# Performance work log

Measured on AMD Instinct MI355X. Metric: run time of the kernel, lower is better.

## Reference

```python
import jax, jax.numpy as jnp
import numpy as np
from jax import lax

D_MODEL = 512
D_STATE = 64
D_CONV = 4
EXPAND = 2
HEADDIM = 64
D_INNER = EXPAND * D_MODEL          # 1024
NHEADS = D_INNER // HEADDIM         # 16
CONV_DIM = D_INNER + 2 * D_STATE    # 1152 (x, B, C go through depthwise conv)
D_PROJ = 2 * D_INNER + 2 * D_STATE + NHEADS  # 2192
EPS = 1e-5


def silu(x):
    return x * jax.nn.sigmoid(x)


def layernorm(x, w, b):
    mu = jnp.mean(x, axis=-1, keepdims=True)
    var = jnp.mean((x - mu) ** 2, axis=-1, keepdims=True)
    return (x - mu) * lax.rsqrt(var + EPS) * w + b


def mamba2(x, in_w, conv_w, conv_b, dt_bias, A_log, D_h, mnorm_w, out_w):
    """Faithful Mamba2 forward (sequential selective-scan form of SSD).
    x: [B, L, D_MODEL]"""
    Bsz, L, _ = x.shape
    zxbcdt = x @ in_w  # [B, L, D_PROJ]
    z = zxbcdt[..., :D_INNER]
    xBC = zxbcdt[..., D_INNER:D_INNER + CONV_DIM]
    dt = zxbcdt[..., -NHEADS:]

    # causal depthwise conv1d over sequence, then SiLU
    xBC_pad = jnp.pad(xBC, ((0, 0), (D_CONV - 1, 0), (0, 0)))
    xBC = lax.conv_general_dilated(
        xBC_pad, conv_w, window_strides=(1,), padding='VALID',
        dimension_numbers=('NWC', 'WIO', 'NWC'), feature_group_count=CONV_DIM)
    xBC = silu(xBC + conv_b)

    xh = xBC[..., :D_INNER].reshape(Bsz, L, NHEADS, HEADDIM)      # [B,L,H,P]
    Bc = xBC[..., D_INNER:D_INNER + D_STATE]                      # [B,L,N]
    Cc = xBC[..., D_INNER + D_STATE:]                             # [B,L,N]

    dt = jax.nn.softplus(dt + dt_bias)          # [B,L,H]
    dA = jnp.exp(dt * (-jnp.exp(A_log)))        # [B,L,H]
    dtx = dt[..., None] * xh                    # [B,L,H,P]

    def step(h, ins):
        dA_t, dtx_t, B_t, C_t = ins  # [B,H], [B,H,P], [B,N], [B,N]
        h = h * dA_t[:, :, None, None] + dtx_t[..., None] * B_t[:, None, None, :]
        y = jnp.einsum('bhpn,bn->bhp', h, C_t)
        return h, y

    h0 = jnp.zeros((Bsz, NHEADS, HEADDIM, D_STATE), x.dtype)
    xs = (jnp.moveaxis(dA, 1, 0), jnp.moveaxis(dtx, 1, 0),
          jnp.moveaxis(Bc, 1, 0), jnp.moveaxis(Cc, 1, 0))
    _, ys = lax.scan(step, h0, xs)              # [L,B,H,P]
    y = jnp.moveaxis(ys, 0, 1) + D_h[None, None, :, None] * xh
    y = y.reshape(Bsz, L, D_INNER)

    # gated RMSNorm: rmsnorm(y * silu(z)) * weight
    g = y * silu(z)
    g = g * lax.rsqrt(jnp.mean(g * g, axis=-1, keepdims=True) + EPS) * mnorm_w
    return g @ out_w  # [B, L, D_MODEL]


def setup_inputs() -> dict:
    key = jax.random.key(0)
    ks = jax.random.split(key, 16)
    B, L = 2, 4096
    s = 0.02
    inp = {
        'x': jax.random.normal(ks[0], (B, L, D_MODEL), jnp.float32),
        'norm_in_w': jnp.ones((D_MODEL,), jnp.float32),
        'norm_in_b': jnp.zeros((D_MODEL,), jnp.float32),
        'norm_out_w': jnp.ones((D_MODEL,), jnp.float32),
        'norm_out_b': jnp.zeros((D_MODEL,), jnp.float32),
        'in_w': jax.random.normal(ks[1], (D_MODEL, D_PROJ), jnp.float32) * s,
        'conv_w': jax.random.normal(ks[2], (D_CONV, 1, CONV_DIM), jnp.float32) * 0.1,
        'conv_b': jnp.zeros((CONV_DIM,), jnp.float32),
        'dt_bias': jnp.log(jnp.expm1(jax.random.uniform(ks[3], (NHEADS,), jnp.float32, 0.001, 0.1))),
        'A_log': jnp.log(jnp.arange(1, NHEADS + 1, dtype=jnp.float32)),
        'D_h': jnp.ones((NHEADS,), jnp.float32),
        'mnorm_w': jnp.ones((D_INNER,), jnp.float32),
        'out_w': jax.random.normal(ks[4], (D_INNER, D_MODEL), jnp.float32) * s,
        'ff_w1': jax.random.normal(ks[5], (D_MODEL, 4 * D_MODEL), jnp.float32) * s,
        'ff_b1': jnp.zeros((4 * D_MODEL,), jnp.float32),
        'ff_w2': jax.random.normal(ks[6], (4 * D_MODEL, D_MODEL), jnp.float32) * s,
        'ff_b2': jnp.zeros((D_MODEL,), jnp.float32),
    }
    return inp


def reference(x, norm_in_w, norm_in_b, norm_out_w, norm_out_b, in_w, conv_w,
              conv_b, dt_bias, A_log, D_h, mnorm_w, out_w, ff_w1, ff_b1,
              ff_w2, ff_b2):
    xn = layernorm(x, norm_in_w, norm_in_b)
    fwd = mamba2(xn, in_w, conv_w, conv_b, dt_bias, A_log, D_h, mnorm_w, out_w)
    bwd = mamba2(jnp.flip(xn, axis=1), in_w, conv_w, conv_b, dt_bias, A_log,
                 D_h, mnorm_w, out_w)
    m = layernorm(fwd + jnp.flip(bwd, axis=1), norm_out_w, norm_out_b)
    ff = jax.nn.gelu(m @ ff_w1 + ff_b1, approximate=False) @ ff_w2 + ff_b2
    return ff + x
```

## Files before the change

kernel.cpp:

```cpp
#include <hip/hip_runtime.h>
#include <hip/hip_bf16.h>

#define LSEQ 4096
#define BSZ 2
#define DMODEL 512
#define DINNER 1024
#define DSTATE 64
#define NHEADS 16
#define CONVDIM 1152
#define DPROJ 2192
#define NPAD 2304
#define NTOK (BSZ*LSEQ)
#define NCH 64

typedef __attribute__((ext_vector_type(8))) short short8;
typedef __attribute__((ext_vector_type(4))) float f32x4;

__device__ inline unsigned short f2b(float v){
  unsigned int u = __builtin_bit_cast(unsigned int, v);
  unsigned int r = (u + 0x7FFFu + ((u >> 16) & 1u)) >> 16;
  return (unsigned short)r;
}
__device__ inline float b2f(unsigned short u){
  unsigned int x = ((unsigned int)u) << 16;
  return __builtin_bit_cast(float, x);
}
__device__ inline uint4 pack8(const float* v){
  uint4 pk;
  pk.x = (unsigned)f2b(v[0]) | ((unsigned)f2b(v[1])<<16);
  pk.y = (unsigned)f2b(v[2]) | ((unsigned)f2b(v[3])<<16);
  pk.z = (unsigned)f2b(v[4]) | ((unsigned)f2b(v[5])<<16);
  pk.w = (unsigned)f2b(v[6]) | ((unsigned)f2b(v[7])<<16);
  return pk;
}
__device__ inline float gelu_f(float x){
  float x2 = x*x;
  float u = x*(0.7978845608f + 0.0356774081f*x2);
  float au = fabsf(u);
  float z = __expf(-2.f*au);
  float t = (1.f - z)/(1.f + z);
  t = (u >= 0.f) ? t : -t;
  return 0.5f*x*(1.f + t);
}

#define GLL16(gp, lp) __builtin_amdgcn_global_load_lds( \
    (const __attribute__((address_space(1))) unsigned int*)(gp), \
    (__attribute__((address_space(3))) unsigned int*)(lp), 16, 0, 0)

__global__ __launch_bounds__(256) void wconv_t(const float* __restrict__ src,
    unsigned short* __restrict__ dst, int K, int Nsrc, int Npad){
  __shared__ float t[32][33];
  int n0 = blockIdx.x*32, k0 = blockIdx.y*32;
  int tx = threadIdx.x & 31, ty = threadIdx.x >> 5;
  for (int i=0;i<4;i++){
    int k = k0 + ty + i*8; int n = n0 + tx;
    t[ty + i*8][tx] = (n < Nsrc) ? src[(size_t)k*Nsrc + n] : 0.f;
  }
  __syncthreads();
  for (int i=0;i<4;i++){
    int n = n0 + ty + i*8; int k = k0 + tx;
    if (n < Npad) dst[(size_t)n*K + k] = f2b(t[tx][ty + i*8]);
  }
}

__global__ __launch_bounds__(256) void layernorm_k(const float* __restrict__ in,
    const float* __restrict__ w, const float* __restrict__ bb, unsigned short* __restrict__ out){
  int row = blockIdx.x; int tid = threadIdx.x;
  const float* r = in + (size_t)row*DMODEL;
  float v0 = r[tid], v1 = r[tid+256];
  float s = v0+v1, sq = v0*v0+v1*v1;
  for (int m=32;m>=1;m>>=1){ s += __shfl_xor(s,m); sq += __shfl_xor(sq,m); }
  __shared__ float ws_[4], wq_[4];
  int wave = tid>>6, lane = tid&63;
  if (lane==0){ ws_[wave]=s; wq_[wave]=sq; }
  __syncthreads();
  s = ws_[0]+ws_[1]+ws_[2]+ws_[3]; sq = wq_[0]+wq_[1]+wq_[2]+wq_[3];
  float mu = s * (1.f/DMODEL);
  float var = sq * (1.f/DMODEL) - mu*mu;
  float rs = rsqrtf(var + 1e-5f);
  out[(size_t)row*DMODEL + tid]     = f2b((v0-mu)*rs*w[tid] + bb[tid]);
  out[(size_t)row*DMODEL + tid+256] = f2b((v1-mu)*rs*w[tid+256] + bb[tid+256]);
}

__global__ __launch_bounds__(256) void layernorm4_k(const float* __restrict__ in0,
    const float* __restrict__ in1, const float* __restrict__ in2, const float* __restrict__ in3,
    const float* __restrict__ w, const float* __restrict__ bb, unsigned short* __restrict__ out){
  int row = blockIdx.x; int tid = threadIdx.x;
  size_t o = (size_t)row*DMODEL;
  float v0 = in0[o+tid] + in1[o+tid] + in2[o+tid] + in3[o+tid];
  float v1 = in0[o+tid+256] + in1[o+tid+256] + in2[o+tid+256] + in3[o+tid+256];
  float s = v0+v1, sq = v0*v0+v1*v1;
  for (int m=32;m>=1;m>>=1){ s += __shfl_xor(s,m); sq += __shfl_xor(sq,m); }
  __shared__ float ws_[4], wq_[4];
  int wave = tid>>6, lane = tid&63;
  if (lane==0){ ws_[wave]=s; wq_[wave]=sq; }
  __syncthreads();
  s = ws_[0]+ws_[1]+ws_[2]+ws_[3]; sq = wq_[0]+wq_[1]+wq_[2]+wq_[3];
  float mu = s * (1.f/DMODEL);
  float var = sq * (1.f/DMODEL) - mu*mu;
  float rs = rsqrtf(var + 1e-5f);
  out[o + tid]     = f2b((v0-mu)*rs*w[tid] + bb[tid]);
  out[o + tid+256] = f2b((v1-mu)*rs*w[tid+256] + bb[tid+256]);
}

__global__ __launch_bounds__(256) void reduce4_k(const float* __restrict__ pa,
    const float* __restrict__ pb, const float* __restrict__ bias,
    const float* __restrict__ resid, float* __restrict__ out){
  const size_t MN4 = (size_t)NTOK*DMODEL/4;
  for (size_t i = (size_t)blockIdx.x*256 + threadIdx.x; i < MN4; i += (size_t)gridDim.x*256){
    float4 a0 = ((const float4*)pa)[i];
    float4 a1 = ((const float4*)pa)[i + MN4];
    float4 b0 = ((const float4*)pb)[i];
    float4 b1 = ((const float4*)pb)[i + MN4];
    float4 rv = ((const float4*)resid)[i];
    int col = (int)((i*4) & (DMODEL-1));
    const float4 bs = *(const float4*)(bias + col);
    float4 o;
    o.x = a0.x + a1.x + b0.x + b1.x + bs.x + rv.x;
    o.y = a0.y + a1.y + b0.y + b1.y + bs.y + rv.y;
    o.z = a0.z + a1.z + b0.z + b1.z + bs.z + rv.z;
    o.w = a0.w + a1.w + b0.w + b1.w + bs.w + rv.w;
    ((float4*)out)[i] = o;
  }
}

__global__ __launch_bounds__(512, 4) void gemm128_k(const unsigned short* __restrict__ A,
    const unsigned short* __restrict__ Bt, void* __restrict__ outp, void* __restrict__ outp_hi,
    int M, int N, int K, int klen, int epi, const float* __restrict__ bias){
  __shared__ __align__(16) unsigned short sm[24576];
  unsigned short* As = sm;
  unsigned short* Bs = sm + 8192;
  const int tid = threadIdx.x;
  const int lane = tid & 63, wave = tid >> 6;
  const int wr = wave >> 2, wc = wave & 3;
  const int l15 = lane & 15, q = lane >> 4;
  int nbx = gridDim.x;
  int bid = blockIdx.y * nbx + blockIdx.x;
  int cpx = (nbx * gridDim.y) >> 3;
  int swz = (bid & 7) * cpx + (bid >> 3);
  int bn = swz % nbx, bm = swz / nbx;
  const int kstart = blockIdx.z * klen;
  const int NT = klen >> 5;
  const int ra  = tid >> 2;
  const int sca = (tid & 3) ^ ((ra >> 1) & 3);
  const int jb1 = tid + 512;
  const int rb1 = jb1 >> 2;
  const int scb1 = (jb1 & 3) ^ ((rb1 >> 1) & 3);
  const unsigned short* ga  = A  + (size_t)(bm*128 + ra )*K + kstart + sca*8;
  const unsigned short* gb0 = Bt + (size_t)(bn*256 + ra )*K + kstart + sca*8;
  const unsigned short* gb1 = Bt + (size_t)(bn*256 + rb1)*K + kstart + scb1*8;
  unsigned short* lAa = As + tid*8;
  unsigned short* lB0 = Bs + tid*8;
  unsigned short* lB1 = Bs + jb1*8;
#define STG(t) { const int go=(t)*32, loa=((t)&1)*4096, lob=((t)&1)*8192; \
  GLL16(ga+go, lAa+loa); GLL16(gb0+go, lB0+lob); GLL16(gb1+go, lB1+lob); }
  f32x4 acc[4][4];
  #pragma unroll
  for (int i=0;i<4;i++)
    #pragma unroll
    for (int j=0;j<4;j++) acc[i][j] = (f32x4){0.f,0.f,0.f,0.f};
  STG(0); STG(1);
  const int cOfs = (q ^ ((l15 >> 1) & 3)) * 8;
  const int arow = wr*64 + l15;
  const int brow = wc*64 + l15;
  for (int t = 0; t < NT; ++t){
    if (t+1 < NT) { asm volatile("s_waitcnt vmcnt(3)" ::: "memory"); }
    else          { asm volatile("s_waitcnt vmcnt(0)" ::: "memory"); }
    __builtin_amdgcn_s_barrier();
    const unsigned short* Ab = As + (t & 1)*4096;
    const unsigned short* Bb = Bs + (t & 1)*8192;
    short8 af[4], bf4[4];
    #pragma unroll
    for (int mt=0;mt<4;mt++) af[mt]  = *(const short8*)(Ab + (arow + mt*16)*32 + cOfs);
    #pragma unroll
    for (int nt=0;nt<4;nt++) bf4[nt] = *(const short8*)(Bb + (brow + nt*16)*32 + cOfs);
    __builtin_amdgcn_s_setprio(1);
    #pragma unroll
    for (int mt=0;mt<4;mt++)
      #pragma unroll
      for (int nt=0;nt<4;nt++)
        acc[mt][nt] = __builtin_amdgcn_mfma_f32_16x16x32_bf16(af[mt], bf4[nt], acc[mt][nt], 0,0,0);
    __builtin_amdgcn_s_setprio(0);
    __builtin_amdgcn_s_barrier();
    if (t+2 < NT) STG(t+2);
  }
#undef STG
  float* cb = (float*)sm + wave*1040;
  const int rbase = q*4;
  const int gr0t = bm*128 + wr*64;
  const int gc0 = bn*256 + wc*64;
  #pragma unroll
  for (int mt=0; mt<4; mt++){
    #pragma unroll
    for (int nt=0;nt<4;nt++)
      #pragma unroll
      for (int r=0;r<4;r++)
        cb[(rbase+r)*65 + nt*16 + l15] = acc[mt][nt][r];
    int gr0 = gr0t + mt*16;
    if (epi == 0){
      float* po = (float*)((blockIdx.z < 2) ? outp : outp_hi)
                + (size_t)(blockIdx.z & 1) * ((size_t)M * N);
      int r4 = lane >> 4, c0f = (lane & 15)*4;
      #pragma unroll
      for (int h=0; h<4; h++){
        int row = h*4 + r4;
        float4 v;
        v.x = cb[row*65 + c0f + 0];
        v.y = cb[row*65 + c0f + 1];
        v.z = cb[row*65 + c0f + 2];
        v.w = cb[row*65 + c0f + 3];
        *(float4*)(po + (size_t)(gr0+row)*N + gc0 + c0f) = v;
      }
    } else {
      int r8 = lane >> 3, c0 = (lane & 7)*8;
      #pragma unroll
      for (int h=0; h<2; h++){
        int row = h*8 + r8;
        float v[8];
        #pragma unroll
        for (int u=0;u<8;u++) v[u] = cb[row*65 + c0 + u];
        if (epi == 1){
          #pragma unroll
          for (int u=0;u<8;u++) v[u] = gelu_f(v[u] + bias[gc0 + c0 + u]);
        }
        *(uint4*)((unsigned short*)outp + (size_t)(gr0+row)*N + gc0 + c0) = pack8(v);
      }
    }
  }
}

__global__ __launch_bounds__(256) void dt_k(const unsigned short* __restrict__ zx,
    const float* __restrict__ dt_bias, const float* __restrict__ A_log,
    float* __restrict__ dAb, float* __restrict__ dtb){
  int b = blockIdx.y;
  int t = blockIdx.x*16 + (threadIdx.x>>4);
  int h = threadIdx.x & 15;
  float raw = b2f(zx[((size_t)b*LSEQ + t)*NPAD + (DINNER+CONVDIM) + h]) + dt_bias[h];
  float dt = (raw > 20.f) ? raw : log1pf(expf(raw));
  float dA = expf(-expf(A_log[h]) * dt);
  size_t f = ((size_t)b*LSEQ + t)*NHEADS + h;
  size_t r = ((size_t)(BSZ+b)*LSEQ + (LSEQ-1-t))*NHEADS + h;
  dAb[f] = dA; dtb[f] = dt;
  dAb[r] = dA; dtb[r] = dt;
}

__global__ __launch_bounds__(256) void conv_x_k(const unsigned short* __restrict__ zx,
    const float* __restrict__ conv_w, const float* __restrict__ conv_b,
    const float* __restrict__ dtb, unsigned short* __restrict__ dtxb,
    unsigned short* __restrict__ zcomp){
  int b = blockIdx.y;
  int t0blk = blockIdx.x * 32;
  int tid = threadIdx.x;
  int half = tid >> 7, cg = tid & 127;
  int c0 = cg * 8;
  int head = c0 >> 6;
  float wk[4][8], bias8[8];
  #pragma unroll
  for (int k=0;k<4;k++)
    #pragma unroll
    for (int j=0;j<8;j++) wk[k][j] = conv_w[k*CONVDIM + c0 + j];
  #pragma unroll
  for (int j=0;j<8;j++) bias8[j] = conv_b[c0 + j];
  __shared__ float sdtf[32][16], sdtb[32][16];
  for (int r = tid; r < 512; r += 256){
    int i = r >> 4, h = r & 15;
    sdtf[i][h] = dtb[((size_t)b*LSEQ + t0blk + i)*NHEADS + h];
    sdtb[i][h] = dtb[((size_t)(BSZ+b)*LSEQ + (LSEQ-1-(t0blk+i)))*NHEADS + h];
  }
  __syncthreads();
  int t0 = t0blk + half*16;
  float w0[8],w1[8],w2[8],w3[8];
  #pragma unroll
  for (int j=0;j<8;j++){ w1[j]=0.f; w2[j]=0.f; w3[j]=0.f; }
  for (int it=0; it<22; ++it){
    int t = t0 - 3 + it;
    #pragma unroll
    for (int j=0;j<8;j++){ w0[j]=w1[j]; w1[j]=w2[j]; w2[j]=w3[j]; }
    if (t >= 0 && t < LSEQ){
      uint4 xv = *(const uint4*)(zx + ((size_t)b*LSEQ + t)*NPAD + DINNER + c0);
      const unsigned short* xs = (const unsigned short*)&xv;
      #pragma unroll
      for (int j=0;j<8;j++) w3[j] = b2f(xs[j]);
      if (t >= t0 && t < t0+16){
        uint4 zv = *(const uint4*)(zx + ((size_t)b*LSEQ + t)*NPAD + c0);
        *(uint4*)(zcomp + ((size_t)b*LSEQ + t)*DINNER + c0) = zv;
      }
    } else {
      #pragma unroll
      for (int j=0;j<8;j++) w3[j] = 0.f;
    }
    if (t >= t0 && t < t0+16){
      float dtf = sdtf[t - t0blk][head];
      float v[8];
      #pragma unroll
      for (int j=0;j<8;j++){
        float a = bias8[j] + wk[0][j]*w0[j] + wk[1][j]*w1[j] + wk[2][j]*w2[j] + wk[3][j]*w3[j];
        v[j] = (a / (1.f + __expf(-a))) * dtf;
      }
      *(uint4*)(dtxb + ((size_t)b*LSEQ + t)*DINNER + c0) = pack8(v);
    }
    int tau = t - 3;
    if (tau >= t0 && tau < t0+16){
      float dtv = sdtb[tau - t0blk][head];
      float v[8];
      #pragma unroll
      for (int j=0;j<8;j++){
        float a = bias8[j] + wk[0][j]*w3[j] + wk[1][j]*w2[j] + wk[2][j]*w1[j] + wk[3][j]*w0[j];
        v[j] = (a / (1.f + __expf(-a))) * dtv;
      }
      *(uint4*)(dtxb + ((size_t)(BSZ+b)*LSEQ + (LSEQ-1-tau))*DINNER + c0) = pack8(v);
    }
  }
}

__global__ __launch_bounds__(256) void conv_bc_k(const unsigned short* __restrict__ zx,
    const float* __restrict__ conv_w, const float* __restrict__ conv_b,
    unsigned short* __restrict__ Bb, unsigned short* __restrict__ Cb){
  int b = blockIdx.y;
  int t0blk = blockIdx.x * 64;
  int tid = threadIdx.x;
  int slot = tid >> 4, cg = tid & 15;
  int c0 = cg*8;
  int ccol = DINNER + 1024 + c0;
  int cw = 1024 + c0;
  float wk[4][8], bias8[8];
  #pragma unroll
  for (int k=0;k<4;k++)
    #pragma unroll
    for (int j=0;j<8;j++) wk[k][j] = conv_w[k*CONVDIM + cw + j];
  #pragma unroll
  for (int j=0;j<8;j++) bias8[j] = conv_b[cw + j];
  int t0 = t0blk + slot*4;
  float w0[8],w1[8],w2[8],w3[8];
  #pragma unroll
  for (int j=0;j<8;j++){ w1[j]=0.f; w2[j]=0.f; w3[j]=0.f; }
  for (int it=0; it<10; ++it){
    int t = t0 - 3 + it;
    #pragma unroll
    for (int j=0;j<8;j++){ w0[j]=w1[j]; w1[j]=w2[j]; w2[j]=w3[j]; }
    if (t >= 0 && t < LSEQ){
      uint4 xv = *(const uint4*)(zx + ((size_t)b*LSEQ + t)*NPAD + ccol);
      const unsigned short* xs = (const unsigned short*)&xv;
      #pragma unroll
      for (int j=0;j<8;j++) w3[j] = b2f(xs[j]);
    } else {
      #pragma unroll
      for (int j=0;j<8;j++) w3[j] = 0.f;
    }
    if (t >= t0 && t < t0+4){
      float v[8];
      #pragma unroll
      for (int j=0;j<8;j++){
        float a = bias8[j] + wk[0][j]*w0[j] + wk[1][j]*w1[j] + wk[2][j]*w2[j] + wk[3][j]*w3[j];
        v[j] = a / (1.f + __expf(-a));
      }
      size_t tok = (size_t)b*LSEQ + t;
      if (c0 < 64) *(uint4*)(Bb + tok*DSTATE + c0)      = pack8(v);
      else         *(uint4*)(Cb + tok*DSTATE + (c0-64)) = pack8(v);
    }
    int tau = t - 3;
    if (tau >= t0 && tau < t0+4){
      float v[8];
      #pragma unroll
      for (int j=0;j<8;j++){
        float a = bias8[j] + wk[0][j]*w3[j] + wk[1][j]*w2[j] + wk[2][j]*w1[j] + wk[3][j]*w0[j];
        v[j] = a / (1.f + __expf(-a));
      }
      size_t tok = (size_t)(BSZ+b)*LSEQ + (LSEQ-1-tau);
      if (c0 < 64) *(uint4*)(Bb + tok*DSTATE + c0)      = pack8(v);
      else         *(uint4*)(Cb + tok*DSTATE + (c0-64)) = pack8(v);
    }
  }
}

template<int SA, int SB>
__device__ inline void gemm64s(const unsigned short* Ab, const unsigned short* Bb_,
                               int l15, int q, f32x4 acc[4][4]){
  #pragma unroll
  for (int ks=0; ks<2; ks++){
    short8 af[4], bf4[4];
    #pragma unroll
    for (int mt=0;mt<4;mt++){
      int r = mt*16 + l15;
      int c = ks*4 + q; if (SA) c ^= (r>>3)&7;
      af[mt] = *(const short8*)(Ab + r*72 + c*8);
    }
    #pragma unroll
    for (int nt=0;nt<4;nt++){
      int r = nt*16 + l15;
      int c = ks*4 + q; if (SB) c ^= (r>>3)&7;
      bf4[nt] = *(const short8*)(Bb_ + r*72 + c*8);
    }
    #pragma unroll
    for (int mt=0;mt<4;mt++)
      #pragma unroll
      for (int nt=0;nt<4;nt++)
        acc[mt][nt] = __builtin_amdgcn_mfma_f32_16x16x32_bf16(af[mt], bf4[nt], acc[mt][nt], 0,0,0);
  }
}
__device__ inline void gemm64(const unsigned short* Ab, const unsigned short* Bb_,
                              int l15, int q, f32x4 acc[4][4]){
  gemm64s<0,0>(Ab, Bb_, l15, q, acc);
}

__global__ __launch_bounds__(64) void ssd1_k(const float* __restrict__ dAb,
    const unsigned short* __restrict__ dtxb, const unsigned short* __restrict__ Bb,
    const unsigned short* __restrict__ Cb,
    unsigned short* __restrict__ y0, unsigned short* __restrict__ y1,
    unsigned short* __restrict__ hbuf, float* __restrict__ Pch, float* __restrict__ ebuf){
  int ch = blockIdx.x, h = blockIdx.y, z = blockIdx.z;
  int d = z >> 1, b = z & 1;
  int lane = threadIdx.x;
  int l15 = lane & 15, q = lane >> 4;
  int tr = lane >> 3, cb8 = (lane & 7)*8;
  int m7 = lane & 7;
  size_t tokb = (size_t)z*LSEQ + (size_t)ch*64;
  size_t zhc = ((size_t)z*NHEADS + h)*NCH + ch;
  __shared__ __align__(16) unsigned short S1[64*72];
  __shared__ __align__(16) unsigned short S2[64*72];
  __shared__ __align__(16) unsigned short S3[64*72];
  __shared__ float Lb[64];
  float L = fmaxf(logf(dAb[(tokb + lane)*NHEADS + h]), -60.f);
  #pragma unroll
  for (int off=1; off<64; off<<=1){
    float v = __shfl_up(L, off);
    if (lane >= off) L += v;
  }
  Lb[lane] = L;
  float e = __expf(L);
  ebuf[zhc*64 + lane] = e;
  if (lane == 63) Pch[zhc] = e;
  for (int i=0;i<8;i++){
    int t = i*8 + tr;
    *(uint4*)&S1[t*72 + cb8] = *(const uint4*)(Cb + (tokb+t)*DSTATE + cb8);
    *(uint4*)&S2[t*72 + cb8] = *(const uint4*)(Bb + (tokb+t)*DSTATE + cb8);
    uint4 xv = *(const uint4*)(dtxb + (tokb+t)*DINNER + (size_t)h*64 + cb8);
    const unsigned short* xs = (const unsigned short*)&xv;
    int csw = ((i ^ m7) << 3) + tr;
    #pragma unroll
    for (int j=0;j<8;j++) S3[(cb8+j)*72 + csw] = xs[j];
  }
  f32x4 sa[4][4];
  for (int i=0;i<4;i++) for (int j=0;j<4;j++) sa[i][j] = (f32x4){0.f,0.f,0.f,0.f};
  gemm64s<0,0>(S1, S2, l15, q, sa);
  float Lsv[4];
  #pragma unroll
  for (int nt=0;nt<4;nt++) Lsv[nt] = Lb[nt*16 + l15];
  int sch = l15 >> 3, sin = l15 & 7;
  #pragma unroll
  for (int mt=0;mt<4;mt++){
    #pragma unroll
    for (int r=0;r<4;r++){
      int t = mt*16 + q*4 + r;
      int trow = (t>>3)&7;
      float Lt = Lb[t];
      #pragma unroll
      for (int nt=0;nt<4;nt++){
        int s = nt*16 + l15;
        float v = (t >= s) ? __expf(Lt - Lsv[nt]) * sa[mt][nt][r] : 0.f;
        S1[t*72 + (((nt*2 + sch) ^ trow)<<3) + sin] = f2b(v);
      }
    }
  }
  f32x4 ya[4][4];
  for (int i=0;i<4;i++) for (int j=0;j<4;j++) ya[i][j] = (f32x4){0.f,0.f,0.f,0.f};
  gemm64s<1,1>(S1, S3, l15, q, ya);
  #pragma unroll
  for (int mt=0;mt<4;mt++)
    #pragma unroll
    for (int pt=0;pt<4;pt++)
      #pragma unroll
      for (int r=0;r<4;r++)
        S2[(mt*16+q*4+r)*72 + pt*16 + l15] = f2b(ya[mt][pt][r]);
  unsigned short* yb = d ? y1 : y0;
  for (int i=0;i<8;i++){
    int t = i*8 + tr; int g = ch*64 + t;
    int tph = d ? (LSEQ-1-g) : g;
    *(uint4*)(yb + ((size_t)b*LSEQ + tph)*DINNER + (size_t)h*64 + cb8) = *(uint4*)&S2[t*72 + cb8];
  }
  float L63 = Lb[63];
  for (int i=0;i<8;i++){
    int s = i*8 + tr;
    float w = __expf(L63 - Lb[s]);
    uint4 bv = *(const uint4*)(Bb + (tokb+s)*DSTATE + cb8);
    const unsigned short* bs = (const unsigned short*)&bv;
    int csw = ((i ^ m7) << 3) + tr;
    #pragma unroll
    for (int j=0;j<8;j++) S2[(cb8+j)*72 + csw] = f2b(w * b2f(bs[j]));
  }
  f32x4 ga[4][4];
  for (int i=0;i<4;i++) for (int j=0;j<4;j++) ga[i][j] = (f32x4){0.f,0.f,0.f,0.f};
  gemm64s<1,1>(S3, S2, l15, q, ga);
  #pragma unroll
  for (int pt=0;pt<4;pt++)
    #pragma unroll
    for (int nt=0;nt<4;nt++)
      #pragma unroll
      for (int r=0;r<4;r++)
        S1[(pt*16+q*4+r)*72 + nt*16 + l15] = f2b(ga[pt][nt][r]);
  for (int i=0;i<8;i++){
    int p = i*8 + tr;
    *(uint4*)(hbuf + zhc*4096 + (size_t)p*64 + cb8) = *(uint4*)&S1[p*72 + cb8];
  }
}

__global__ __launch_bounds__(256) void comb_k(unsigned short* __restrict__ hbuf,
    const float* __restrict__ Pch){
  int u = blockIdx.x; int tid = threadIdx.x;
  int kb = blockIdx.y * 4;
  size_t base0 = ((size_t)u*NCH)*4096;
  float hreg[4];
  unsigned short ccur[4], cnxt[4] = {0,0,0,0};
  #pragma unroll
  for (int k=0;k<4;k++){ hreg[k]=0.f; ccur[k] = hbuf[base0 + tid + (size_t)(kb+k)*256]; }
  float Pc = Pch[(size_t)u*NCH], Pn = 0.f;
  for (int ch=0; ch<NCH; ch++){
    size_t base = base0 + (size_t)ch*4096;
    if (ch+1 < NCH){
      size_t bnx = base + 4096;
      #pragma unroll
      for (int k=0;k<4;k++) cnxt[k] = hbuf[bnx + tid + (size_t)(kb+k)*256];
      Pn = Pch[(size_t)u*NCH + ch + 1];
    }
    #pragma unroll
    for (int k=0;k<4;k++){
      hbuf[base + tid + (size_t)(kb+k)*256] = f2b(hreg[k]);
      hreg[k] = hreg[k]*Pc + b2f(ccur[k]);
    }
    #pragma unroll
    for (int k=0;k<4;k++) ccur[k] = cnxt[k];
    Pc = Pn;
  }
}

__global__ __launch_bounds__(64) void ssd2_k(const unsigned short* __restrict__ Cb,
    const unsigned short* __restrict__ hbuf, const unsigned short* __restrict__ dtxb,
    const float* __restrict__ dtb, const float* __restrict__ ebuf, const float* __restrict__ Dh,
    unsigned short* __restrict__ y0, unsigned short* __restrict__ y1){
  int ch = blockIdx.x, h = blockIdx.y, z = blockIdx.z;
  int d = z >> 1, b = z & 1;
  int lane = threadIdx.x;
  int l15 = lane & 15, q = lane >> 4;
  int tr = lane >> 3, cb8 = (lane & 7)*8;
  size_t tokb = (size_t)z*LSEQ + (size_t)ch*64;
  size_t zhc = ((size_t)z*NHEADS + h)*NCH + ch;
  __shared__ __align__(16) unsigned short S1[64*72];
  __shared__ __align__(16) unsigned short S2[64*72];
  __shared__ __align__(16) unsigned short S3[64*72];
  __shared__ float eb2[64], dti[64];
  eb2[lane] = ebuf[zhc*64 + lane];
  dti[lane] = 1.f / dtb[(tokb + lane)*NHEADS + h];
  float Dv = Dh[h];
  for (int i=0;i<8;i++){
    int t = i*8 + tr;
    *(uint4*)&S1[t*72 + cb8] = *(const uint4*)(Cb + (tokb+t)*DSTATE + cb8);
    *(uint4*)&S2[t*72 + cb8] = *(const uint4*)(hbuf + zhc*4096 + (size_t)t*64 + cb8);
  }
  f32x4 acc[4][4];
  for (int i=0;i<4;i++) for (int j=0;j<4;j++) acc[i][j] = (f32x4){0.f,0.f,0.f,0.f};
  gemm64(S1, S2, l15, q, acc);
  unsigned short* yb = d ? y1 : y0;
  #pragma unroll
  for (int mt=0;mt<4;mt++){
    #pragma unroll
    for (int r=0;r<4;r++){
      int t = mt*16 + q*4 + r; int g = ch*64 + t;
      int tph = d ? (LSEQ-1-g) : g;
      size_t rowb = ((size_t)b*LSEQ + tph)*DINNER + (size_t)h*64;
      size_t dxb_ = (tokb + t)*DINNER + (size_t)h*64;
      float et = eb2[t], di = dti[t];
      #pragma unroll
      for (int pt=0;pt<4;pt++){
        int p = pt*16 + l15;
        float v = acc[mt][pt][r]*et + b2f(yb[rowb + p]) + Dv * b2f(dtxb[dxb_ + p]) * di;
        S3[t*72 + p] = f2b(v);
      }
    }
  }
  for (int i=0;i<8;i++){
    int t = i*8 + tr; int g = ch*64 + t;
    int tph = d ? (LSEQ-1-g) : g;
    *(uint4*)(yb + ((size_t)b*LSEQ + tph)*DINNER + (size_t)h*64 + cb8) = *(uint4*)&S3[t*72 + cb8];
  }
}

__global__ __launch_bounds__(256) void gate_k(const unsigned short* __restrict__ y0,
    const unsigned short* __restrict__ y1, const unsigned short* __restrict__ zcomp,
    const float* __restrict__ mnw, unsigned short* __restrict__ gsum){
  int tok = blockIdx.x; int tid = threadIdx.x;
  __shared__ float g0s[DINNER], g1s[DINNER];
  float ss0 = 0.f, ss1 = 0.f;
  for (int i=0;i<4;i++){
    int c = tid + i*256;
    float z = b2f(zcomp[(size_t)tok*DINNER + c]);
    float sz = z / (1.f + __expf(-z));
    float g0 = b2f(y0[(size_t)tok*DINNER + c]) * sz;
    float g1 = b2f(y1[(size_t)tok*DINNER + c]) * sz;
    g0s[c] = g0; g1s[c] = g1;
    ss0 += g0*g0; ss1 += g1*g1;
  }
  for (int m=32;m>=1;m>>=1){ ss0 += __shfl_xor(ss0,m); ss1 += __shfl_xor(ss1,m); }
  __shared__ float w0[4], w1[4];
  int wave = tid>>6, lane = tid&63;
  if (lane==0){ w0[wave]=ss0; w1[wave]=ss1; }
  __syncthreads();
  ss0 = w0[0]+w0[1]+w0[2]+w0[3];
  ss1 = w1[0]+w1[1]+w1[2]+w1[3];
  float r0 = rsqrtf(ss0*(1.f/DINNER) + 1e-5f);
  float r1 = rsqrtf(ss1*(1.f/DINNER) + 1e-5f);
  for (int i=0;i<4;i++){
    int c = tid + i*256;
    gsum[(size_t)tok*DINNER + c] = f2b((g0s[c]*r0 + g1s[c]*r1) * mnw[c]);
  }
}

extern "C" void kernel_launch(void* const* d_in, const int* in_sizes, int n_in,
                              void* d_out, int out_size, void* d_ws, size_t ws_size,
                              hipStream_t stream){
  const float* x       = (const float*)d_in[0];
  const float* nin_w   = (const float*)d_in[1];
  const float* nin_b   = (const float*)d_in[2];
  const float* nout_w  = (const float*)d_in[3];
  const float* nout_b  = (const float*)d_in[4];
  const float* in_w    = (const float*)d_in[5];
  const float* conv_w  = (const float*)d_in[6];
  const float* conv_b  = (const float*)d_in[7];
  const float* dt_bias = (const float*)d_in[8];
  const float* A_log   = (const float*)d_in[9];
  const float* D_h     = (const float*)d_in[10];
  const float* mnorm_w = (const float*)d_in[11];
  const float* out_w   = (const float*)d_in[12];
  const float* ff_w1   = (const float*)d_in[13];
  const float* ff_b1   = (const float*)d_in[14];
  const float* ff_w2   = (const float*)d_in[15];
  const float* ff_b2   = (const float*)d_in[16];
  float* out = (float*)d_out;

  char* ws = (char*)d_ws;
  size_t off = 0;
  auto alloc = [&](size_t bytes)->char*{
    char* p = ws + off; off = (off + bytes + 255) & ~(size_t)255; return p; };
  unsigned short* xn_bf = (unsigned short*)alloc((size_t)NTOK*DMODEL*2);
  unsigned short* in_wT = (unsigned short*)alloc((size_t)NPAD*DMODEL*2);
  unsigned short* out_wT= (unsigned short*)alloc((size_t)DMODEL*DINNER*2);
  unsigned short* w1T   = (unsigned short*)alloc((size_t)2048*DMODEL*2);
  unsigned short* w2T   = (unsigned short*)alloc((size_t)DMODEL*2048*2);
  unsigned short* zx    = (unsigned short*)alloc((size_t)NTOK*NPAD*2);
  unsigned short* zcomp = (unsigned short*)alloc((size_t)NTOK*DINNER*2);
  float*          dAb   = (float*)alloc((size_t)2*NTOK*NHEADS*4);
  float*          dtb   = (float*)alloc((size_t)2*NTOK*NHEADS*4);
  unsigned short* Bb    = (unsigned short*)alloc((size_t)2*NTOK*DSTATE*2);
  unsigned short* Cb    = (unsigned short*)alloc((size_t)2*NTOK*DSTATE*2);
  unsigned short* dtxb  = (unsigned short*)alloc((size_t)2*NTOK*DINNER*2);
  unsigned short* y0    = (unsigned short*)alloc((size_t)NTOK*DINNER*2);
  unsigned short* y1    = (unsigned short*)alloc((size_t)NTOK*DINNER*2);
  float*          Pch   = (float*)alloc((size_t)64*NCH*4);
  float*          ebuf  = (float*)alloc((size_t)64*NCH*64*4);
  size_t need = off;
  if (need > ws_size) return;

  unsigned short* hbuf  = zx;
  unsigned short* gsum  = dtxb;
  float* mp01 = (float*)zx;
  float* mp23 = (float*)y0;
  unsigned short* m_bf  = xn_bf;
  unsigned short* h1    = zx;
  float* fp01 = (float*)dtxb;
  float* fp23 = (float*)y0;

  wconv_t<<<dim3(NPAD/32,   DMODEL/32), 256, 0, stream>>>(in_w,  in_wT,  DMODEL, DPROJ,  NPAD);
  wconv_t<<<dim3(DMODEL/32, DINNER/32), 256, 0, stream>>>(out_w, out_wT, DINNER, DMODEL, DMODEL);
  wconv_t<<<dim3(2048/32,   DMODEL/32), 256, 0, stream>>>(ff_w1, w1T,    DMODEL, 2048,   2048);
  wconv_t<<<dim3(DMODEL/32, 2048/32),   256, 0, stream>>>(ff_w2, w2T,    2048,   DMODEL, DMODEL);
  layernorm_k<<<NTOK, 256, 0, stream>>>(x, nin_w, nin_b, xn_bf);
  gemm128_k<<<dim3(NPAD/256, NTOK/128, 1), 512, 0, stream>>>(xn_bf, in_wT, zx, nullptr, NTOK, NPAD, DMODEL, DMODEL, 3, nullptr);
  dt_k<<<dim3(LSEQ/16, BSZ), 256, 0, stream>>>(zx, dt_bias, A_log, dAb, dtb);
  conv_x_k<<<dim3(LSEQ/32, BSZ), 256, 0, stream>>>(zx, conv_w, conv_b, dtb, dtxb, zcomp);
  conv_bc_k<<<dim3(LSEQ/64, BSZ), 256, 0, stream>>>(zx, conv_w, conv_b, Bb, Cb);
  ssd1_k<<<dim3(NCH, NHEADS, 2*BSZ), 64, 0, stream>>>(dAb, dtxb, Bb, Cb, y0, y1, hbuf, Pch, ebuf);
  comb_k<<<dim3(64, 4), 256, 0, stream>>>(hbuf, Pch);
  ssd2_k<<<dim3(NCH, NHEADS, 2*BSZ), 64, 0, stream>>>(Cb, hbuf, dtxb, dtb, ebuf, D_h, y0, y1);
  gate_k<<<NTOK, 256, 0, stream>>>(y0, y1, zcomp, mnorm_w, gsum);
  gemm128_k<<<dim3(DMODEL/256, NTOK/128, 4), 512, 0, stream>>>(gsum, out_wT, mp01, mp23, NTOK, DMODEL, DINNER, 256, 0, nullptr);
  layernorm4_k<<<NTOK, 256, 0, stream>>>(mp01, mp01 + (size_t)NTOK*DMODEL, mp23, mp23 + (size_t)NTOK*DMODEL, nout_w, nout_b, m_bf);
  gemm128_k<<<dim3(2048/256, NTOK/128, 1), 512, 0, stream>>>(m_bf, w1T, h1, nullptr, NTOK, 2048, DMODEL, DMODEL, 1, ff_b1);
  gemm128_k<<<dim3(DMODEL/256, NTOK/128, 4), 512, 0, stream>>>(h1, w2T, fp01, fp23, NTOK, DMODEL, 2048, 512, 0, nullptr);
  reduce4_k<<<2048, 256, 0, stream>>>(fp01, fp23, ff_b2, x, out);
}
```

Measured before the change: 398.7 us.

## Split SSD chunk kernels across four wavefronts per block

The intra-chunk SSD kernels ssd1_k and ssd2_k move from one 64-lane wavefront per block to four wavefronts. Each wave computes one 16-column slice of every 64x64 MFMA product, and the loads and stores are shared across waves, with __syncthreads between stages. This cuts the per-wave accumulator registers and serial work, so each chunk has more parallelism and more latency hiding. In exchange it adds barrier overhead and the waves reload the A fragments redundantly.

```diff
diff --git a/kernel.cpp b/kernel.cpp
--- a/kernel.cpp
+++ b/kernel.cpp
@@ -374,43 +374,37 @@
 }
 
 template<int SA, int SB>
-__device__ inline void gemm64s(const unsigned short* Ab, const unsigned short* Bb_,
-                               int l15, int q, f32x4 acc[4][4]){
+__device__ inline void gemm64w(const unsigned short* Ab, const unsigned short* Bb_,
+                               int l15, int q, int nt, f32x4 acc[4]){
   #pragma unroll
   for (int ks=0; ks<2; ks++){
-    short8 af[4], bf4[4];
+    short8 af[4], bf;
     #pragma unroll
     for (int mt=0;mt<4;mt++){
       int r = mt*16 + l15;
       int c = ks*4 + q; if (SA) c ^= (r>>3)&7;
       af[mt] = *(const short8*)(Ab + r*72 + c*8);
     }
-    #pragma unroll
-    for (int nt=0;nt<4;nt++){
+    {
       int r = nt*16 + l15;
       int c = ks*4 + q; if (SB) c ^= (r>>3)&7;
-      bf4[nt] = *(const short8*)(Bb_ + r*72 + c*8);
+      bf = *(const short8*)(Bb_ + r*72 + c*8);
     }
     #pragma unroll
     for (int mt=0;mt<4;mt++)
-      #pragma unroll
-      for (int nt=0;nt<4;nt++)
-        acc[mt][nt] = __builtin_amdgcn_mfma_f32_16x16x32_bf16(af[mt], bf4[nt], acc[mt][nt], 0,0,0);
-  }
-}
-__device__ inline void gemm64(const unsigned short* Ab, const unsigned short* Bb_,
-                              int l15, int q, f32x4 acc[4][4]){
-  gemm64s<0,0>(Ab, Bb_, l15, q, acc);
-}
-
-__global__ __launch_bounds__(64) void ssd1_k(const float* __restrict__ dAb,
+      acc[mt] = __builtin_amdgcn_mfma_f32_16x16x32_bf16(af[mt], bf, acc[mt], 0,0,0);
+  }
+}
+
+__global__ __launch_bounds__(256) void ssd1_k(const float* __restrict__ dAb,
     const unsigned short* __restrict__ dtxb, const unsigned short* __restrict__ Bb,
     const unsigned short* __restrict__ Cb,
     unsigned short* __restrict__ y0, unsigned short* __restrict__ y1,
     unsigned short* __restrict__ hbuf, float* __restrict__ Pch, float* __restrict__ ebuf){
   int ch = blockIdx.x, h = blockIdx.y, z = blockIdx.z;
   int d = z >> 1, b = z & 1;
-  int lane = threadIdx.x;
+  int tid = threadIdx.x;
+  int lane = tid & 63, w = tid >> 6;
   int l15 = lane & 15, q = lane >> 4;
   int tr = lane >> 3, cb8 = (lane & 7)*8;
   int m7 = lane & 7;
@@ -426,12 +420,15 @@
     float v = __shfl_up(L, off);
     if (lane >= off) L += v;
   }
-  Lb[lane] = L;
-  float e = __expf(L);
-  ebuf[zhc*64 + lane] = e;
-  if (lane == 63) Pch[zhc] = e;
-  for (int i=0;i<8;i++){
-    int t = i*8 + tr;
+  if (w == 0){
+    Lb[lane] = L;
+    float e = __expf(L);
+    ebuf[zhc*64 + lane] = e;
+    if (lane == 63) Pch[zhc] = e;
+  }
+  #pragma unroll
+  for (int ii=0; ii<2; ii++){
+    int i = w*2 + ii; int t = i*8 + tr;
     *(uint4*)&S1[t*72 + cb8] = *(const uint4*)(Cb + (tokb+t)*DSTATE + cb8);
     *(uint4*)&S2[t*72 + cb8] = *(const uint4*)(Bb + (tokb+t)*DSTATE + cb8);
     uint4 xv = *(const uint4*)(dtxb + (tokb+t)*DINNER + (size_t)h*64 + cb8);
@@ -440,12 +437,13 @@
     #pragma unroll
     for (int j=0;j<8;j++) S3[(cb8+j)*72 + csw] = xs[j];
   }
-  f32x4 sa[4][4];
-  for (int i=0;i<4;i++) for (int j=0;j<4;j++) sa[i][j] = (f32x4){0.f,0.f,0.f,0.f};
-  gemm64s<0,0>(S1, S2, l15, q, sa);
-  float Lsv[4];
-  #pragma unroll
-  for (int nt=0;nt<4;nt++) Lsv[nt] = Lb[nt*16 + l15];
+  __syncthreads();
+  f32x4 sa[4];
+  #pragma unroll
+  for (int i=0;i<4;i++) sa[i] = (f32x4){0.f,0.f,0.f,0.f};
+  gemm64w<0,0>(S1, S2, l15, q, w, sa);
+  float Lsv = Lb[w*16 + l15];
+  __syncthreads();
   int sch = l15 >> 3, sin = l15 & 7;
   #pragma unroll
   for (int mt=0;mt<4;mt++){
@@ -454,52 +452,55 @@
       int t = mt*16 + q*4 + r;
       int trow = (t>>3)&7;
       float Lt = Lb[t];
-      #pragma unroll
-      for (int nt=0;nt<4;nt++){
-        int s = nt*16 + l15;
-        float v = (t >= s) ? __expf(Lt - Lsv[nt]) * sa[mt][nt][r] : 0.f;
-        S1[t*72 + (((nt*2 + sch) ^ trow)<<3) + sin] = f2b(v);
-      }
-    }
-  }
-  f32x4 ya[4][4];
-  for (int i=0;i<4;i++) for (int j=0;j<4;j++) ya[i][j] = (f32x4){0.f,0.f,0.f,0.f};
-  gemm64s<1,1>(S1, S3, l15, q, ya);
+      int s = w*16 + l15;
+      float v = (t >= s) ? __expf(Lt - Lsv) * sa[mt][r] : 0.f;
+      S1[t*72 + (((w*2 + sch) ^ trow)<<3) + sin] = f2b(v);
+    }
+  }
+  __syncthreads();
+  f32x4 ya[4];
+  #pragma unroll
+  for (int i=0;i<4;i++) ya[i] = (f32x4){0.f,0.f,0.f,0.f};
+  gemm64w<1,1>(S1, S3, l15, q, w, ya);
   #pragma unroll
   for (int mt=0;mt<4;mt++)
     #pragma unroll
-    for (int pt=0;pt<4;pt++)
-      #pragma unroll
-      for (int r=0;r<4;r++)
-        S2[(mt*16+q*4+r)*72 + pt*16 + l15] = f2b(ya[mt][pt][r]);
+    for (int r=0;r<4;r++)
+      S2[(mt*16+q*4+r)*72 + w*16 + l15] = f2b(ya[mt][r]);
+  __syncthreads();
   unsigned short* yb = d ? y1 : y0;
-  for (int i=0;i<8;i++){
-    int t = i*8 + tr; int g = ch*64 + t;
+  #pragma unroll
+  for (int ii=0; ii<2; ii++){
+    int i = w*2 + ii; int t = i*8 + tr; int g = ch*64 + t;
     int tph = d ? (LSEQ-1-g) : g;
     *(uint4*)(yb + ((size_t)b*LSEQ + tph)*DINNER + (size_t)h*64 + cb8) = *(uint4*)&S2[t*72 + cb8];
   }
+  __syncthreads();
   float L63 = Lb[63];
-  for (int i=0;i<8;i++){
-    int s = i*8 + tr;
-    float w = __expf(L63 - Lb[s]);
+  #pragma unroll
+  for (int ii=0; ii<2; ii++){
+    int i = w*2 + ii; int s = i*8 + tr;
+    float wgt = __expf(L63 - Lb[s]);
     uint4 bv = *(const uint4*)(Bb + (tokb+s)*DSTATE + cb8);
     const unsigned short* bs = (const unsigned short*)&bv;
     int csw = ((i ^ m7) << 3) + tr;
     #pragma unroll
-    for (int j=0;j<8;j++) S2[(cb8+j)*72 + csw] = f2b(w * b2f(bs[j]));
-  }
-  f32x4 ga[4][4];
-  for (int i=0;i<4;i++) for (int j=0;j<4;j++) ga[i][j] = (f32x4){0.f,0.f,0.f,0.f};
-  gemm64s<1,1>(S3, S2, l15, q, ga);
+    for (int j=0;j<8;j++) S2[(cb8+j)*72 + csw] = f2b(wgt * b2f(bs[j]));
+  }
+  __syncthreads();
+  f32x4 ga[4];
+  #pragma unroll
+  for (int i=0;i<4;i++) ga[i] = (f32x4){0.f,0.f,0.f,0.f};
+  gemm64w<1,1>(S3, S2, l15, q, w, ga);
   #pragma unroll
   for (int pt=0;pt<4;pt++)
     #pragma unroll
-    for (int nt=0;nt<4;nt++)
-      #pragma unroll
-      for (int r=0;r<4;r++)
-        S1[(pt*16+q*4+r)*72 + nt*16 + l15] = f2b(ga[pt][nt][r]);
-  for (int i=0;i<8;i++){
-    int p = i*8 + tr;
+    for (int r=0;r<4;r++)
+      S1[(pt*16+q*4+r)*72 + w*16 + l15] = f2b(ga[pt][r]);
+  __syncthreads();
+  #pragma unroll
+  for (int ii=0; ii<2; ii++){
+    int i = w*2 + ii; int p = i*8 + tr;
     *(uint4*)(hbuf + zhc*4096 + (size_t)p*64 + cb8) = *(uint4*)&S1[p*72 + cb8];
   }
 }
@@ -533,13 +534,14 @@
   }
 }
 
-__global__ __launch_bounds__(64) void ssd2_k(const unsigned short* __restrict__ Cb,
+__global__ __launch_bounds__(256) void ssd2_k(const unsigned short* __restrict__ Cb,
     const unsigned short* __restrict__ hbuf, const unsigned short* __restrict__ dtxb,
     const float* __restrict__ dtb, const float* __restrict__ ebuf, const float* __restrict__ Dh,
     unsigned short* __restrict__ y0, unsigned short* __restrict__ y1){
   int ch = blockIdx.x, h = blockIdx.y, z = blockIdx.z;
   int d = z >> 1, b = z & 1;
-  int lane = threadIdx.x;
+  int tid = threadIdx.x;
+  int lane = tid & 63, w = tid >> 6;
   int l15 = lane & 15, q = lane >> 4;
   int tr = lane >> 3, cb8 = (lane & 7)*8;
   size_t tokb = (size_t)z*LSEQ + (size_t)ch*64;
@@ -548,17 +550,22 @@
   __shared__ __align__(16) unsigned short S2[64*72];
   __shared__ __align__(16) unsigned short S3[64*72];
   __shared__ float eb2[64], dti[64];
-  eb2[lane] = ebuf[zhc*64 + lane];
-  dti[lane] = 1.f / dtb[(tokb + lane)*NHEADS + h];
+  if (w == 0){
+    eb2[lane] = ebuf[zhc*64 + lane];
+    dti[lane] = 1.f / dtb[(tokb + lane)*NHEADS + h];
+  }
   float Dv = Dh[h];
-  for (int i=0;i<8;i++){
-    int t = i*8 + tr;
+  #pragma unroll
+  for (int ii=0; ii<2; ii++){
+    int i = w*2 + ii; int t = i*8 + tr;
     *(uint4*)&S1[t*72 + cb8] = *(const uint4*)(Cb + (tokb+t)*DSTATE + cb8);
     *(uint4*)&S2[t*72 + cb8] = *(const uint4*)(hbuf + zhc*4096 + (size_t)t*64 + cb8);
   }
-  f32x4 acc[4][4];
-  for (int i=0;i<4;i++) for (int j=0;j<4;j++) acc[i][j] = (f32x4){0.f,0.f,0.f,0.f};
-  gemm64(S1, S2, l15, q, acc);
+  __syncthreads();
+  f32x4 acc[4];
+  #pragma unroll
+  for (int i=0;i<4;i++) acc[i] = (f32x4){0.f,0.f,0.f,0.f};
+  gemm64w<0,0>(S1, S2, l15, q, w, acc);
   unsigned short* yb = d ? y1 : y0;
   #pragma unroll
   for (int mt=0;mt<4;mt++){
@@ -569,16 +576,15 @@
       size_t rowb = ((size_t)b*LSEQ + tph)*DINNER + (size_t)h*64;
       size_t dxb_ = (tokb + t)*DINNER + (size_t)h*64;
       float et = eb2[t], di = dti[t];
-      #pragma unroll
-      for (int pt=0;pt<4;pt++){
-        int p = pt*16 + l15;
-        float v = acc[mt][pt][r]*et + b2f(yb[rowb + p]) + Dv * b2f(dtxb[dxb_ + p]) * di;
-        S3[t*72 + p] = f2b(v);
-      }
-    }
-  }
-  for (int i=0;i<8;i++){
-    int t = i*8 + tr; int g = ch*64 + t;
+      int p = w*16 + l15;
+      float v = acc[mt][r]*et + b2f(yb[rowb + p]) + Dv * b2f(dtxb[dxb_ + p]) * di;
+      S3[t*72 + p] = f2b(v);
+    }
+  }
+  __syncthreads();
+  #pragma unroll
+  for (int ii=0; ii<2; ii++){
+    int i = w*2 + ii; int t = i*8 + tr; int g = ch*64 + t;
     int tph = d ? (LSEQ-1-g) : g;
     *(uint4*)(yb + ((size_t)b*LSEQ + tph)*DINNER + (size_t)h*64 + cb8) = *(uint4*)&S3[t*72 + cb8];
   }
@@ -677,9 +683,9 @@
   dt_k<<<dim3(LSEQ/16, BSZ), 256, 0, stream>>>(zx, dt_bias, A_log, dAb, dtb);
   conv_x_k<<<dim3(LSEQ/32, BSZ), 256, 0, stream>>>(zx, conv_w, conv_b, dtb, dtxb, zcomp);
   conv_bc_k<<<dim3(LSEQ/64, BSZ), 256, 0, stream>>>(zx, conv_w, conv_b, Bb, Cb);
-  ssd1_k<<<dim3(NCH, NHEADS, 2*BSZ), 64, 0, stream>>>(dAb, dtxb, Bb, Cb, y0, y1, hbuf, Pch, ebuf);
+  ssd1_k<<<dim3(NCH, NHEADS, 2*BSZ), 256, 0, stream>>>(dAb, dtxb, Bb, Cb, y0, y1, hbuf, Pch, ebuf);
   comb_k<<<dim3(64, 4), 256, 0, stream>>>(hbuf, Pch);
-  ssd2_k<<<dim3(NCH, NHEADS, 2*BSZ), 64, 0, stream>>>(Cb, hbuf, dtxb, dtb, ebuf, D_h, y0, y1);
+  ssd2_k<<<dim3(NCH, NHEADS, 2*BSZ), 256, 0, stream>>>(Cb, hbuf, dtxb, dtb, ebuf, D_h, y0, y1);
   gate_k<<<NTOK, 256, 0, stream>>>(y0, y1, zcomp, mnorm_w, gsum);
   gemm128_k<<<dim3(DMODEL/256, NTOK/128, 4), 512, 0, stream>>>(gsum, out_wT, mp01, mp23, NTOK, DMODEL, DINNER, 256, 0, nullptr);
   layernorm4_k<<<NTOK, 256, 0, stream>>>(mp01, mp01 + (size_t)NTOK*DMODEL, mp23, mp23 + (size_t)NTOK*DMODEL, nout_w, nout_b, m_bf);
```

After: 367.0 us, median of 2. 1.09x faster.
